# Kernel optimization log

Measured on AMD Instinct MI355X. Metric: run time of the kernel, lower is better.

The kernel has to match this reference:

```python
import jax, jax.numpy as jnp
import numpy as np
import math

B, H, L = 8, 256, 4096
C = 1            # channels
D_STATE = 64
DD = D_STATE // 2  # d = 32
DT_MIN, DT_MAX = 1e-3, 1e-1


def setup_inputs() -> dict:
    key = jax.random.key(0)
    ks = jax.random.split(key, 6)
    u = jax.random.normal(ks[0], (B, H, L), dtype=jnp.float32)
    # analytic init matching the torch module
    h_scale = jnp.exp(jnp.arange(H, dtype=jnp.float32) / H * math.log(DT_MAX / DT_MIN))  # (H,)
    angles = jnp.arange(DD, dtype=jnp.float32) * jnp.float32(np.pi)                      # (DD,)
    theta = jnp.einsum('c,h,d->chd', jnp.ones((C,), jnp.float32), h_scale, angles)       # (C,H,DD)
    a = -jnp.broadcast_to(h_scale[None, :, None], (C, H, DD)).astype(jnp.float32)        # (C,H,DD)
    D = jax.random.normal(ks[1], (C, H), dtype=jnp.float32)
    b_p = jax.random.normal(ks[2], (C, H, DD), dtype=jnp.float32)
    c_p = jax.random.normal(ks[3], (C, H, DD), dtype=jnp.float32)
    x0 = jax.random.normal(ks[4], (C, H, DD), dtype=jnp.float32)
    return {"u": u, "theta": theta, "a": a, "D": D, "b_p": b_p, "c_p": c_p, "x0": x0}


def fft_conv(u, f):
    # u: (B,H,L), f: (C,H,L) -> (B,C,H,L) causal conv via zero-padded FFT
    l = u.shape[-1]
    n = 2 * l
    u_f = jnp.fft.rfft(u, n=n)          # (B,H,n//2+1)
    f_f = jnp.fft.rfft(f, n=n)          # (C,H,n//2+1)
    y_f = jnp.einsum('bhl,chl->bchl', u_f, f_f)
    return jnp.fft.irfft(y_f, n=n)[..., :l]


def reference(u, theta, a, D, b_p, c_p, x0):
    l = u.shape[-1]
    T = 1.0 / (l - 1)
    zk = T * jnp.arange(l, dtype=jnp.float32)            # (L,)
    zk4 = zk[None, None, :, None]                         # (1,1,L,1)
    ls = -jnp.abs(a) + 1j * theta                         # (C,H,DD) complex
    term_0 = (jnp.exp(ls * T) - 1.0) / ls                 # (C,H,DD)
    # base_term: (C,H,L,DD)
    base_term = (2.0 * term_0[:, :, None, :] * jnp.exp(ls[:, :, None, :] * zk4)).real
    q = b_p * c_p                                         # (C,H,DD)
    f = jnp.einsum('chd,chld->chl', q, base_term)         # (C,H,L)
    y = fft_conv(u, f)                                    # (B,C,H,L)
    y = y + jnp.einsum('bhl,ch->bchl', u, D)
    # initial-condition term
    cos_term = 2.0 * T * jnp.exp(-jnp.abs(a)[:, :, None, :] * zk4) * jnp.cos(theta[:, :, None, :] * zk4)
    init = jnp.einsum('chd,chld->chl', 2.0 * (c_p * x0), cos_term)  # (C,H,L)
    y = y + init[None]                                    # broadcast over batch
    b = y.shape[0]
    return y.reshape(b, -1, l)                            # (B, C*H, L)
```

## Files before the change

kernel.cpp:

```cpp
#include <hip/hip_runtime.h>

#define BB 8
#define HH 256
#define LL 4096
#define STR 72

#define WS_H  0
#define WS_P  (2u*1024*1024)
#define WS_R  (4u*1024*1024)
#define WS_C1 (6u*1024*1024)
#define WS_C2 (6u*1024*1024 + 128u*1024)

typedef __attribute__((ext_vector_type(8))) short short8;
typedef __attribute__((ext_vector_type(4))) float f32x4;

static __device__ inline unsigned short f2bf(float x) {
    union { float f; unsigned u; } v; v.f = x;
    unsigned r = v.u + 0x7fffu + ((v.u >> 16) & 1u);
    return (unsigned short)(r >> 16);
}
static __device__ inline float bf2f(unsigned short us) {
    union { unsigned u; float f; } v; v.u = ((unsigned)us) << 16; return v.f;
}

#define CMUL(or_, oi_, ar_, ai_, br_, bi_) do { \
    float _tr = fmaf((ar_), (br_), -(ai_) * (bi_)); \
    float _ti = fmaf((ar_), (bi_), (ai_) * (br_)); \
    (or_) = _tr; (oi_) = _ti; } while (0)

__global__ __launch_bounds__(256) void s4_pre_kernel(
    const float* __restrict__ theta, const float* __restrict__ a,
    const float* __restrict__ b_p,   const float* __restrict__ c_p,
    const float* __restrict__ x0,
    unsigned short* __restrict__ Hm, unsigned short* __restrict__ Pm,
    unsigned short* __restrict__ Rm, float4* __restrict__ C1,
    float* __restrict__ C2)
{
    const int tid = threadIdx.x;
    const int h   = blockIdx.x;
    const int d   = tid & 31;
    const int kb  = tid >> 5;
    const float T = 1.0f / (LL - 1);
    __shared__ float h_s[64];

    const float lr = a[h * 32 + d];
    const float li = theta[h * 32 + d];
    float sn, cS;
    sincosf(li * T, &sn, &cS);
    const float er = expf(lr * T);
    const float Rr = er * cS, Ri = er * sn;
    const float den = lr * lr + li * li;
    const float t0r = ((Rr - 1.f) * lr + Ri * li) / den;
    const float t0i = (Ri * lr - (Rr - 1.f) * li) / den;
    const float qq  = b_p[h * 32 + d] * c_p[h * 32 + d];
    const float wre = 2.f * qq * t0r, wim = 2.f * qq * t0i;
    const float vv  = 4.f * T * c_p[h * 32 + d] * x0[h * 32 + d];

    float r2r, r2i, r4r, r4i, r8r, r8i, r16r, r16i, r32r, r32i;
    CMUL(r2r, r2i, Rr, Ri, Rr, Ri);
    CMUL(r4r, r4i, r2r, r2i, r2r, r2i);
    CMUL(r8r, r8i, r4r, r4i, r4r, r4i);
    CMUL(r16r, r16i, r8r, r8i, r8r, r8i);
    CMUL(r32r, r32i, r16r, r16i, r16r, r16i);

    unsigned short* HmB = Hm + h * 4096;
    unsigned short* PmB = Pm + h * 4096;
    unsigned short* RmB = Rm + h * 4096;

    {
        float pr = 1.f, pi = 0.f;
        if (kb & 1) CMUL(pr, pi, pr, pi, r8r, r8i);
        if (kb & 2) CMUL(pr, pi, pr, pi, r16r, r16i);
        if (kb & 4) CMUL(pr, pi, pr, pi, r32r, r32i);
        #pragma unroll
        for (int k8 = 0; k8 < 8; ++k8) {
            const int k = (kb << 3) + k8;
            RmB[k * 64 + d]           = f2bf(pr);
            RmB[k * 64 + 32 + d]      = f2bf(-pi);
            PmB[d * 64 + (63 - k)]        = f2bf(pr);
            PmB[(32 + d) * 64 + (63 - k)] = f2bf(pi);
            float hk = fmaf(wre, pr, -wim * pi);
            hk += __shfl_xor(hk, 1);
            hk += __shfl_xor(hk, 2);
            hk += __shfl_xor(hk, 4);
            hk += __shfl_xor(hk, 8);
            hk += __shfl_xor(hk, 16);
            if (d == 0) h_s[k] = hk;
            CMUL(pr, pi, pr, pi, Rr, Ri);
        }
    }
    if (tid < 32) {
        float Ar, Ai, wrr, wri;
        CMUL(Ar, Ai, r32r, r32i, r32r, r32i);
        CMUL(wrr, wri, wre, wim, Rr, Ri);
        C1[h * 32 + d] = make_float4(Ar, Ai, wrr, wri);
        C2[h * 32 + d] = vv;
    }
    __syncthreads();

    {
        const int t  = tid >> 2;
        const int tb = (tid & 3) << 4;
        #pragma unroll
        for (int g = 0; g < 4; ++g) {
            const int tau0 = tb + (g << 2);
            unsigned short e[4];
            #pragma unroll
            for (int i = 0; i < 4; ++i) {
                const int dt = t - (tau0 + i);
                e[i] = (dt >= 0) ? f2bf(h_s[dt]) : (unsigned short)0;
            }
            uint2 pk;
            pk.x = (unsigned)e[0] | ((unsigned)e[1] << 16);
            pk.y = (unsigned)e[2] | ((unsigned)e[3] << 16);
            *(uint2*)&HmB[t * 64 + tau0] = pk;
        }
    }
}

__global__ __launch_bounds__(256, 5) void s4_main_kernel(
    const float* __restrict__ u, const float* __restrict__ Dp,
    const unsigned short* __restrict__ Hm, const unsigned short* __restrict__ Pm,
    const unsigned short* __restrict__ Rm, const float4* __restrict__ C1,
    const float* __restrict__ C2, float* __restrict__ out)
{
    const int tid = threadIdx.x;
    const int bh  = blockIdx.x;
    const int hh  = bh & (HH - 1);

    __shared__ __align__(16) short Us[64 * STR];
    __shared__ __align__(16) short EQ[64 * STR];
    __shared__ __align__(16) float Seg[32 * 18];

    const float* up = u + ((size_t)bh << 12);
    #pragma unroll
    for (int jj = 0; jj < 4; ++jj) {
        const int v  = tid + (jj << 8);
        const float4 val = ((const float4*)up)[v];
        const int c  = v >> 4;
        const int t0 = (v & 15) << 2;
        uint2 pk;
        pk.x = (unsigned)f2bf(val.x) | ((unsigned)f2bf(val.y) << 16);
        pk.y = (unsigned)f2bf(val.z) | ((unsigned)f2bf(val.w) << 16);
        *(uint2*)&Us[c * STR + t0] = pk;
    }

    const int d = tid & 31;
    const int g = tid >> 5;
    const float4 c1 = C1[hh * 32 + d];
    const float vv  = C2[hh * 32 + d];
    const float Dh  = Dp[hh];
    __syncthreads();

    const int ln   = tid & 63;
    const int m0   = (tid >> 6) << 4;
    const int rowi = ln & 15;
    const int quad = ln >> 4;
    const unsigned short* HmB = Hm + hh * 4096;
    const unsigned short* PmB = Pm + hh * 4096;
    const unsigned short* RmB = Rm + hh * 4096;
    f32x4 accY[4], accE[4];
    #pragma unroll
    for (int nt = 0; nt < 4; ++nt) {
        accY[nt] = (f32x4){0.f, 0.f, 0.f, 0.f};
        accE[nt] = (f32x4){0.f, 0.f, 0.f, 0.f};
    }
    #pragma unroll
    for (int k0 = 0; k0 < 64; k0 += 32) {
        const short8 aH = *(const short8*)&HmB[(m0 + rowi) * 64 + k0 + (quad << 3)];
        const short8 aP = *(const short8*)&PmB[(m0 + rowi) * 64 + k0 + (quad << 3)];
        #pragma unroll
        for (int nt = 0; nt < 4; ++nt) {
            const short8 bU = *(const short8*)&Us[((nt << 4) + rowi) * STR + k0 + (quad << 3)];
            accY[nt] = __builtin_amdgcn_mfma_f32_16x16x32_bf16(aH, bU, accY[nt], 0, 0, 0);
            accE[nt] = __builtin_amdgcn_mfma_f32_16x16x32_bf16(aP, bU, accE[nt], 0, 0, 0);
        }
    }

    #pragma unroll
    for (int nt = 0; nt < 4; ++nt) {
        uint2 pk;
        pk.x = (unsigned)f2bf(accE[nt][0]) | ((unsigned)f2bf(accE[nt][1]) << 16);
        pk.y = (unsigned)f2bf(accE[nt][2]) | ((unsigned)f2bf(accE[nt][3]) << 16);
        *(uint2*)&EQ[((nt << 4) + rowi) * STR + m0 + (quad << 2)] = pk;
    }
    __syncthreads();

    const float Ar = c1.x, Ai = c1.y;
    float Er[8], Ei[8];
    {
        float Sr = 0.f, Si = 0.f;
        #pragma unroll
        for (int i = 0; i < 8; ++i) {
            const int c = (g << 3) + i;
            Er[i] = bf2f((unsigned short)EQ[c * STR + d]);
            Ei[i] = bf2f((unsigned short)EQ[c * STR + 32 + d]);
            const float nr = fmaf(Ar, Sr, fmaf(-Ai, Si, Er[i]));
            const float ni = fmaf(Ar, Si, fmaf(Ai, Sr, Ei[i]));
            Sr = nr; Si = ni;
        }
        Seg[d * 18 + (g << 1)]     = Sr;
        Seg[d * 18 + (g << 1) + 1] = Si;
    }
    __syncthreads();

    {
        float S8r, S8i, S16r, S16i, S32r, S32i;
        float b1r, b1i, b2r, b2i;
        CMUL(b1r, b1i, Ar, Ai, Ar, Ai);
        CMUL(b2r, b2i, b1r, b1i, b1r, b1i);
        CMUL(S8r, S8i, b2r, b2i, b2r, b2i);
        CMUL(S16r, S16i, S8r, S8i, S8r, S8i);
        CMUL(S32r, S32i, S16r, S16i, S16r, S16i);
        float offr = 0.f, offi = 0.f;
        #pragma unroll
        for (int gp = 0; gp < 7; ++gp) {
            const float2 sg = *(const float2*)&Seg[d * 18 + (gp << 1)];
            const float nr = fmaf(S8r, offr, fmaf(-S8i, offi, sg.x));
            const float ni = fmaf(S8r, offi, fmaf(S8i, offr, sg.y));
            const bool take = gp < g;
            offr = take ? nr : offr;
            offi = take ? ni : offi;
        }
        float Gr = vv, Gi = 0.f;
        if (g & 1) { float nr, ni; CMUL(nr, ni, Gr, Gi, S8r, S8i);   Gr = nr; Gi = ni; }
        if (g & 2) { float nr, ni; CMUL(nr, ni, Gr, Gi, S16r, S16i); Gr = nr; Gi = ni; }
        if (g & 4) { float nr, ni; CMUL(nr, ni, Gr, Gi, S32r, S32i); Gr = nr; Gi = ni; }
        const float wrr = c1.z, wri = c1.w;
        float Sr = offr, Si = offi;
        #pragma unroll
        for (int i = 0; i < 8; ++i) {
            const int c = (g << 3) + i;
            const float Qr = fmaf(wrr, Sr, fmaf(-wri, Si, Gr));
            const float Qi = fmaf(wrr, Si, fmaf(wri, Sr, Gi));
            EQ[c * STR + d]      = (short)f2bf(Qr);
            EQ[c * STR + 32 + d] = (short)f2bf(Qi);
            const float nr = fmaf(Ar, Sr, fmaf(-Ai, Si, Er[i]));
            const float ni = fmaf(Ar, Si, fmaf(Ai, Sr, Ei[i]));
            Sr = nr; Si = ni;
            float nGr, nGi;
            CMUL(nGr, nGi, Ar, Ai, Gr, Gi);
            Gr = nGr; Gi = nGi;
        }
    }
    __syncthreads();

    #pragma unroll
    for (int k0 = 0; k0 < 64; k0 += 32) {
        const short8 aR = *(const short8*)&RmB[(m0 + rowi) * 64 + k0 + (quad << 3)];
        #pragma unroll
        for (int nt = 0; nt < 4; ++nt) {
            const short8 bQ = *(const short8*)&EQ[((nt << 4) + rowi) * STR + k0 + (quad << 3)];
            accY[nt] = __builtin_amdgcn_mfma_f32_16x16x32_bf16(aR, bQ, accY[nt], 0, 0, 0);
        }
    }

    float* op = out + ((size_t)bh << 12);
    #pragma unroll
    for (int nt = 0; nt < 4; ++nt) {
        const int c    = (nt << 4) + rowi;
        const int toff = m0 + (quad << 2);
        const uint2 uu = *(const uint2*)&Us[c * STR + toff];
        float4 res;
        res.x = fmaf(Dh, bf2f((unsigned short)(uu.x & 0xffffu)), accY[nt][0]);
        res.y = fmaf(Dh, bf2f((unsigned short)(uu.x >> 16)),     accY[nt][1]);
        res.z = fmaf(Dh, bf2f((unsigned short)(uu.y & 0xffffu)), accY[nt][2]);
        res.w = fmaf(Dh, bf2f((unsigned short)(uu.y >> 16)),     accY[nt][3]);
        *(float4*)&op[c * 64 + toff] = res;
    }
}

extern "C" void kernel_launch(void* const* d_in, const int* in_sizes, int n_in,
                              void* d_out, int out_size, void* d_ws, size_t ws_size,
                              hipStream_t stream) {
    const float* u     = (const float*)d_in[0];
    const float* theta = (const float*)d_in[1];
    const float* a     = (const float*)d_in[2];
    const float* Dp    = (const float*)d_in[3];
    const float* b_p   = (const float*)d_in[4];
    const float* c_p   = (const float*)d_in[5];
    const float* x0    = (const float*)d_in[6];
    float* out = (float*)d_out;
    char* ws = (char*)d_ws;
    unsigned short* Hm = (unsigned short*)(ws + WS_H);
    unsigned short* Pm = (unsigned short*)(ws + WS_P);
    unsigned short* Rm = (unsigned short*)(ws + WS_R);
    float4*         C1 = (float4*)(ws + WS_C1);
    float*          C2 = (float*)(ws + WS_C2);

    hipLaunchKernelGGL(s4_pre_kernel, dim3(HH), dim3(256), 0, stream,
                       theta, a, b_p, c_p, x0, Hm, Pm, Rm, C1, C2);
    hipLaunchKernelGGL(s4_main_kernel, dim3(BB * HH), dim3(256), 0, stream,
                       u, Dp, Hm, Pm, Rm, C1, C2, out);
}
```

Before: 105.1 us.

## Process two batch rows per block, reuse H/P/R fragments and prefetch second input

```diff
diff --git a/kernel.cpp b/kernel.cpp
--- a/kernel.cpp
+++ b/kernel.cpp
@@ -118,155 +118,193 @@
     }
 }
 
-__global__ __launch_bounds__(256, 5) void s4_main_kernel(
+__global__ __launch_bounds__(256, 4) void s4_main_kernel(
     const float* __restrict__ u, const float* __restrict__ Dp,
     const unsigned short* __restrict__ Hm, const unsigned short* __restrict__ Pm,
     const unsigned short* __restrict__ Rm, const float4* __restrict__ C1,
     const float* __restrict__ C2, float* __restrict__ out)
 {
     const int tid = threadIdx.x;
-    const int bh  = blockIdx.x;
-    const int hh  = bh & (HH - 1);
-
-    __shared__ __align__(16) short Us[64 * STR];
+    const int blk = blockIdx.x;
+    const int hh  = blk >> 2;
+    const int bp  = blk & 3;
+
+    __shared__ __align__(16) short UsA[64 * STR];
+    __shared__ __align__(16) short UsB[64 * STR];
     __shared__ __align__(16) short EQ[64 * STR];
     __shared__ __align__(16) float Seg[32 * 18];
 
-    const float* up = u + ((size_t)bh << 12);
+    const int d    = tid & 31;
+    const int g    = tid >> 5;
+    const int ln   = tid & 63;
+    const int m0   = (tid >> 6) << 4;
+    const int rowi = ln & 15;
+    const int quad = ln >> 4;
+
+    const unsigned short* HmB = Hm + hh * 4096;
+    const unsigned short* PmB = Pm + hh * 4096;
+    const unsigned short* RmB = Rm + hh * 4096;
+    short8 aH[2], aP[2], aR[2];
+    #pragma unroll
+    for (int kh = 0; kh < 2; ++kh) {
+        const int off = (m0 + rowi) * 64 + (kh << 5) + (quad << 3);
+        aH[kh] = *(const short8*)&HmB[off];
+        aP[kh] = *(const short8*)&PmB[off];
+        aR[kh] = *(const short8*)&RmB[off];
+    }
+
+    const float* up0 = u + ((((size_t)(bp * 2) * HH) + hh) << 12);
+    const float* up1 = u + ((((size_t)(bp * 2 + 1) * HH) + hh) << 12);
     #pragma unroll
     for (int jj = 0; jj < 4; ++jj) {
         const int v  = tid + (jj << 8);
-        const float4 val = ((const float4*)up)[v];
+        const float4 val = ((const float4*)up0)[v];
         const int c  = v >> 4;
         const int t0 = (v & 15) << 2;
         uint2 pk;
         pk.x = (unsigned)f2bf(val.x) | ((unsigned)f2bf(val.y) << 16);
         pk.y = (unsigned)f2bf(val.z) | ((unsigned)f2bf(val.w) << 16);
-        *(uint2*)&Us[c * STR + t0] = pk;
-    }
-
-    const int d = tid & 31;
-    const int g = tid >> 5;
+        *(uint2*)&UsA[c * STR + t0] = pk;
+    }
+    float4 v1[4];
+    #pragma unroll
+    for (int jj = 0; jj < 4; ++jj)
+        v1[jj] = ((const float4*)up1)[tid + (jj << 8)];
+
     const float4 c1 = C1[hh * 32 + d];
     const float vv  = C2[hh * 32 + d];
     const float Dh  = Dp[hh];
-    __syncthreads();
-
-    const int ln   = tid & 63;
-    const int m0   = (tid >> 6) << 4;
-    const int rowi = ln & 15;
-    const int quad = ln >> 4;
-    const unsigned short* HmB = Hm + hh * 4096;
-    const unsigned short* PmB = Pm + hh * 4096;
-    const unsigned short* RmB = Rm + hh * 4096;
-    f32x4 accY[4], accE[4];
-    #pragma unroll
-    for (int nt = 0; nt < 4; ++nt) {
-        accY[nt] = (f32x4){0.f, 0.f, 0.f, 0.f};
-        accE[nt] = (f32x4){0.f, 0.f, 0.f, 0.f};
-    }
-    #pragma unroll
-    for (int k0 = 0; k0 < 64; k0 += 32) {
-        const short8 aH = *(const short8*)&HmB[(m0 + rowi) * 64 + k0 + (quad << 3)];
-        const short8 aP = *(const short8*)&PmB[(m0 + rowi) * 64 + k0 + (quad << 3)];
-        #pragma unroll
-        for (int nt = 0; nt < 4; ++nt) {
-            const short8 bU = *(const short8*)&Us[((nt << 4) + rowi) * STR + k0 + (quad << 3)];
-            accY[nt] = __builtin_amdgcn_mfma_f32_16x16x32_bf16(aH, bU, accY[nt], 0, 0, 0);
-            accE[nt] = __builtin_amdgcn_mfma_f32_16x16x32_bf16(aP, bU, accE[nt], 0, 0, 0);
-        }
-    }
-
-    #pragma unroll
-    for (int nt = 0; nt < 4; ++nt) {
-        uint2 pk;
-        pk.x = (unsigned)f2bf(accE[nt][0]) | ((unsigned)f2bf(accE[nt][1]) << 16);
-        pk.y = (unsigned)f2bf(accE[nt][2]) | ((unsigned)f2bf(accE[nt][3]) << 16);
-        *(uint2*)&EQ[((nt << 4) + rowi) * STR + m0 + (quad << 2)] = pk;
-    }
-    __syncthreads();
-
     const float Ar = c1.x, Ai = c1.y;
-    float Er[8], Ei[8];
+    float S8r, S8i, S16r, S16i, S32r, S32i;
     {
-        float Sr = 0.f, Si = 0.f;
-        #pragma unroll
-        for (int i = 0; i < 8; ++i) {
-            const int c = (g << 3) + i;
-            Er[i] = bf2f((unsigned short)EQ[c * STR + d]);
-            Ei[i] = bf2f((unsigned short)EQ[c * STR + 32 + d]);
-            const float nr = fmaf(Ar, Sr, fmaf(-Ai, Si, Er[i]));
-            const float ni = fmaf(Ar, Si, fmaf(Ai, Sr, Ei[i]));
-            Sr = nr; Si = ni;
-        }
-        Seg[d * 18 + (g << 1)]     = Sr;
-        Seg[d * 18 + (g << 1) + 1] = Si;
-    }
-    __syncthreads();
-
-    {
-        float S8r, S8i, S16r, S16i, S32r, S32i;
         float b1r, b1i, b2r, b2i;
         CMUL(b1r, b1i, Ar, Ai, Ar, Ai);
         CMUL(b2r, b2i, b1r, b1i, b1r, b1i);
         CMUL(S8r, S8i, b2r, b2i, b2r, b2i);
         CMUL(S16r, S16i, S8r, S8i, S8r, S8i);
         CMUL(S32r, S32i, S16r, S16i, S16r, S16i);
-        float offr = 0.f, offi = 0.f;
-        #pragma unroll
-        for (int gp = 0; gp < 7; ++gp) {
-            const float2 sg = *(const float2*)&Seg[d * 18 + (gp << 1)];
-            const float nr = fmaf(S8r, offr, fmaf(-S8i, offi, sg.x));
-            const float ni = fmaf(S8r, offi, fmaf(S8i, offr, sg.y));
-            const bool take = gp < g;
-            offr = take ? nr : offr;
-            offi = take ? ni : offi;
-        }
-        float Gr = vv, Gi = 0.f;
-        if (g & 1) { float nr, ni; CMUL(nr, ni, Gr, Gi, S8r, S8i);   Gr = nr; Gi = ni; }
-        if (g & 2) { float nr, ni; CMUL(nr, ni, Gr, Gi, S16r, S16i); Gr = nr; Gi = ni; }
-        if (g & 4) { float nr, ni; CMUL(nr, ni, Gr, Gi, S32r, S32i); Gr = nr; Gi = ni; }
-        const float wrr = c1.z, wri = c1.w;
-        float Sr = offr, Si = offi;
-        #pragma unroll
-        for (int i = 0; i < 8; ++i) {
-            const int c = (g << 3) + i;
-            const float Qr = fmaf(wrr, Sr, fmaf(-wri, Si, Gr));
-            const float Qi = fmaf(wrr, Si, fmaf(wri, Sr, Gi));
-            EQ[c * STR + d]      = (short)f2bf(Qr);
-            EQ[c * STR + 32 + d] = (short)f2bf(Qi);
-            const float nr = fmaf(Ar, Sr, fmaf(-Ai, Si, Er[i]));
-            const float ni = fmaf(Ar, Si, fmaf(Ai, Sr, Ei[i]));
-            Sr = nr; Si = ni;
-            float nGr, nGi;
-            CMUL(nGr, nGi, Ar, Ai, Gr, Gi);
-            Gr = nGr; Gi = nGi;
-        }
     }
     __syncthreads();
 
     #pragma unroll
-    for (int k0 = 0; k0 < 64; k0 += 32) {
-        const short8 aR = *(const short8*)&RmB[(m0 + rowi) * 64 + k0 + (quad << 3)];
+    for (int it = 0; it < 2; ++it) {
+        short* Us = it ? UsB : UsA;
+
+        f32x4 accY[4], accE[4];
         #pragma unroll
         for (int nt = 0; nt < 4; ++nt) {
-            const short8 bQ = *(const short8*)&EQ[((nt << 4) + rowi) * STR + k0 + (quad << 3)];
-            accY[nt] = __builtin_amdgcn_mfma_f32_16x16x32_bf16(aR, bQ, accY[nt], 0, 0, 0);
-        }
-    }
-
-    float* op = out + ((size_t)bh << 12);
-    #pragma unroll
-    for (int nt = 0; nt < 4; ++nt) {
-        const int c    = (nt << 4) + rowi;
-        const int toff = m0 + (quad << 2);
-        const uint2 uu = *(const uint2*)&Us[c * STR + toff];
-        float4 res;
-        res.x = fmaf(Dh, bf2f((unsigned short)(uu.x & 0xffffu)), accY[nt][0]);
-        res.y = fmaf(Dh, bf2f((unsigned short)(uu.x >> 16)),     accY[nt][1]);
-        res.z = fmaf(Dh, bf2f((unsigned short)(uu.y & 0xffffu)), accY[nt][2]);
-        res.w = fmaf(Dh, bf2f((unsigned short)(uu.y >> 16)),     accY[nt][3]);
-        *(float4*)&op[c * 64 + toff] = res;
+            accY[nt] = (f32x4){0.f, 0.f, 0.f, 0.f};
+            accE[nt] = (f32x4){0.f, 0.f, 0.f, 0.f};
+        }
+        #pragma unroll
+        for (int kh = 0; kh < 2; ++kh) {
+            const int k0 = kh << 5;
+            #pragma unroll
+            for (int nt = 0; nt < 4; ++nt) {
+                const short8 bU = *(const short8*)&Us[((nt << 4) + rowi) * STR + k0 + (quad << 3)];
+                accY[nt] = __builtin_amdgcn_mfma_f32_16x16x32_bf16(aH[kh], bU, accY[nt], 0, 0, 0);
+                accE[nt] = __builtin_amdgcn_mfma_f32_16x16x32_bf16(aP[kh], bU, accE[nt], 0, 0, 0);
+            }
+        }
+
+        #pragma unroll
+        for (int nt = 0; nt < 4; ++nt) {
+            uint2 pk;
+            pk.x = (unsigned)f2bf(accE[nt][0]) | ((unsigned)f2bf(accE[nt][1]) << 16);
+            pk.y = (unsigned)f2bf(accE[nt][2]) | ((unsigned)f2bf(accE[nt][3]) << 16);
+            *(uint2*)&EQ[((nt << 4) + rowi) * STR + m0 + (quad << 2)] = pk;
+        }
+
+        if (it == 0) {
+            #pragma unroll
+            for (int jj = 0; jj < 4; ++jj) {
+                const int v  = tid + (jj << 8);
+                const int c  = v >> 4;
+                const int t0 = (v & 15) << 2;
+                uint2 pk;
+                pk.x = (unsigned)f2bf(v1[jj].x) | ((unsigned)f2bf(v1[jj].y) << 16);
+                pk.y = (unsigned)f2bf(v1[jj].z) | ((unsigned)f2bf(v1[jj].w) << 16);
+                *(uint2*)&UsB[c * STR + t0] = pk;
+            }
+        }
+        __syncthreads();
+
+        const int cb = g << 3;
+        float Er[8], Ei[8];
+        {
+            float Sr = 0.f, Si = 0.f;
+            #pragma unroll
+            for (int i = 0; i < 8; ++i) {
+                const int c = cb + i;
+                Er[i] = bf2f((unsigned short)EQ[c * STR + d]);
+                Ei[i] = bf2f((unsigned short)EQ[c * STR + 32 + d]);
+                const float nr = fmaf(Ar, Sr, fmaf(-Ai, Si, Er[i]));
+                const float ni = fmaf(Ar, Si, fmaf(Ai, Sr, Ei[i]));
+                Sr = nr; Si = ni;
+            }
+            Seg[d * 18 + (g << 1)]     = Sr;
+            Seg[d * 18 + (g << 1) + 1] = Si;
+        }
+        __syncthreads();
+
+        {
+            float offr = 0.f, offi = 0.f;
+            #pragma unroll
+            for (int gp = 0; gp < 7; ++gp) {
+                const float2 sg = *(const float2*)&Seg[d * 18 + (gp << 1)];
+                const float nr = fmaf(S8r, offr, fmaf(-S8i, offi, sg.x));
+                const float ni = fmaf(S8r, offi, fmaf(S8i, offr, sg.y));
+                const bool take = gp < g;
+                offr = take ? nr : offr;
+                offi = take ? ni : offi;
+            }
+            float Gr = vv, Gi = 0.f;
+            if (g & 1) { float nr, ni; CMUL(nr, ni, Gr, Gi, S8r, S8i);   Gr = nr; Gi = ni; }
+            if (g & 2) { float nr, ni; CMUL(nr, ni, Gr, Gi, S16r, S16i); Gr = nr; Gi = ni; }
+            if (g & 4) { float nr, ni; CMUL(nr, ni, Gr, Gi, S32r, S32i); Gr = nr; Gi = ni; }
+            const float wrr = c1.z, wri = c1.w;
+            float Sr = offr, Si = offi;
+            #pragma unroll
+            for (int i = 0; i < 8; ++i) {
+                const int c = cb + i;
+                const float Qr = fmaf(wrr, Sr, fmaf(-wri, Si, Gr));
+                const float Qi = fmaf(wrr, Si, fmaf(wri, Sr, Gi));
+                EQ[c * STR + d]      = (short)f2bf(Qr);
+                EQ[c * STR + 32 + d] = (short)f2bf(Qi);
+                const float nr = fmaf(Ar, Sr, fmaf(-Ai, Si, Er[i]));
+                const float ni = fmaf(Ar, Si, fmaf(Ai, Sr, Ei[i]));
+                Sr = nr; Si = ni;
+                float nGr, nGi;
+                CMUL(nGr, nGi, Ar, Ai, Gr, Gi);
+                Gr = nGr; Gi = nGi;
+            }
+        }
+        __syncthreads();
+
+        #pragma unroll
+        for (int kh = 0; kh < 2; ++kh) {
+            const int k0 = kh << 5;
+            #pragma unroll
+            for (int nt = 0; nt < 4; ++nt) {
+                const short8 bQ = *(const short8*)&EQ[((nt << 4) + rowi) * STR + k0 + (quad << 3)];
+                accY[nt] = __builtin_amdgcn_mfma_f32_16x16x32_bf16(aR[kh], bQ, accY[nt], 0, 0, 0);
+            }
+        }
+
+        float* op = out + ((((size_t)(bp * 2 + it) * HH) + hh) << 12);
+        #pragma unroll
+        for (int nt = 0; nt < 4; ++nt) {
+            const int c    = (nt << 4) + rowi;
+            const int toff = m0 + (quad << 2);
+            const uint2 uu = *(const uint2*)&Us[c * STR + toff];
+            float4 res;
+            res.x = fmaf(Dh, bf2f((unsigned short)(uu.x & 0xffffu)), accY[nt][0]);
+            res.y = fmaf(Dh, bf2f((unsigned short)(uu.x >> 16)),     accY[nt][1]);
+            res.z = fmaf(Dh, bf2f((unsigned short)(uu.y & 0xffffu)), accY[nt][2]);
+            res.w = fmaf(Dh, bf2f((unsigned short)(uu.y >> 16)),     accY[nt][3]);
+            *(float4*)&op[c * 64 + toff] = res;
+        }
+        __syncthreads();
     }
 }
 
@@ -290,6 +328,6 @@
 
     hipLaunchKernelGGL(s4_pre_kernel, dim3(HH), dim3(256), 0, stream,
                        theta, a, b_p, c_p, x0, Hm, Pm, Rm, C1, C2);
-    hipLaunchKernelGGL(s4_main_kernel, dim3(BB * HH), dim3(256), 0, stream,
+    hipLaunchKernelGGL(s4_main_kernel, dim3(HH * 4), dim3(256), 0, stream,
                        u, Dp, Hm, Pm, Rm, C1, C2, out);
 }
```

After: 104.6 us. No clear change (-0.5%).

## Map one wavefront per (batch, head) sequence and fold D skip into Toeplitz diagonal

Applied to the files above, without the earlier changes.

```diff
diff --git a/kernel.cpp b/kernel.cpp
--- a/kernel.cpp
+++ b/kernel.cpp
@@ -1,6 +1,5 @@
 #include <hip/hip_runtime.h>
 
-#define BB 8
 #define HH 256
 #define LL 4096
 #define STR 72
@@ -31,7 +30,7 @@
 __global__ __launch_bounds__(256) void s4_pre_kernel(
     const float* __restrict__ theta, const float* __restrict__ a,
     const float* __restrict__ b_p,   const float* __restrict__ c_p,
-    const float* __restrict__ x0,
+    const float* __restrict__ x0,    const float* __restrict__ Dp,
     unsigned short* __restrict__ Hm, unsigned short* __restrict__ Pm,
     unsigned short* __restrict__ Rm, float4* __restrict__ C1,
     float* __restrict__ C2)
@@ -45,6 +44,7 @@
 
     const float lr = a[h * 32 + d];
     const float li = theta[h * 32 + d];
+    const float Dh = Dp[h];
     float sn, cS;
     sincosf(li * T, &sn, &cS);
     const float er = expf(lr * T);
@@ -75,8 +75,8 @@
         #pragma unroll
         for (int k8 = 0; k8 < 8; ++k8) {
             const int k = (kb << 3) + k8;
-            RmB[k * 64 + d]           = f2bf(pr);
-            RmB[k * 64 + 32 + d]      = f2bf(-pi);
+            RmB[k * 64 + (d << 1)]     = f2bf(pr);
+            RmB[k * 64 + (d << 1) + 1] = f2bf(-pi);
             PmB[d * 64 + (63 - k)]        = f2bf(pr);
             PmB[(32 + d) * 64 + (63 - k)] = f2bf(pi);
             float hk = fmaf(wre, pr, -wim * pi);
@@ -85,7 +85,7 @@
             hk += __shfl_xor(hk, 4);
             hk += __shfl_xor(hk, 8);
             hk += __shfl_xor(hk, 16);
-            if (d == 0) h_s[k] = hk;
+            if (d == 0) h_s[k] = hk + ((k == 0) ? Dh : 0.f);
             CMUL(pr, pi, pr, pi, Rr, Ri);
         }
     }
@@ -118,156 +118,161 @@
     }
 }
 
-__global__ __launch_bounds__(256, 5) void s4_main_kernel(
-    const float* __restrict__ u, const float* __restrict__ Dp,
+__global__ __launch_bounds__(256, 2) void s4_main_kernel(
+    const float* __restrict__ u,
     const unsigned short* __restrict__ Hm, const unsigned short* __restrict__ Pm,
     const unsigned short* __restrict__ Rm, const float4* __restrict__ C1,
     const float* __restrict__ C2, float* __restrict__ out)
 {
-    const int tid = threadIdx.x;
-    const int bh  = blockIdx.x;
-    const int hh  = bh & (HH - 1);
-
-    __shared__ __align__(16) short Us[64 * STR];
-    __shared__ __align__(16) short EQ[64 * STR];
-    __shared__ __align__(16) float Seg[32 * 18];
-
-    const float* up = u + ((size_t)bh << 12);
-    #pragma unroll
-    for (int jj = 0; jj < 4; ++jj) {
-        const int v  = tid + (jj << 8);
-        const float4 val = ((const float4*)up)[v];
-        const int c  = v >> 4;
-        const int t0 = (v & 15) << 2;
-        uint2 pk;
-        pk.x = (unsigned)f2bf(val.x) | ((unsigned)f2bf(val.y) << 16);
-        pk.y = (unsigned)f2bf(val.z) | ((unsigned)f2bf(val.w) << 16);
-        *(uint2*)&Us[c * STR + t0] = pk;
-    }
-
-    const int d = tid & 31;
-    const int g = tid >> 5;
+    const int tid   = threadIdx.x;
+    const int ln    = tid & 63;
+    const int wslot = tid >> 6;
+    const int wv    = (blockIdx.x << 2) + wslot;
+    const int hh    = wv >> 3;
+    const int b     = wv & 7;
+    const int rowi  = ln & 15;
+    const int quad  = ln >> 4;
+    const int d     = ln & 31;
+    const int half  = ln >> 5;
+
+    __shared__ __align__(16) short lds[4 * 64 * STR];
+    short* Tt = lds + wslot * (64 * STR);
+
     const float4 c1 = C1[hh * 32 + d];
     const float vv  = C2[hh * 32 + d];
-    const float Dh  = Dp[hh];
-    __syncthreads();
-
-    const int ln   = tid & 63;
-    const int m0   = (tid >> 6) << 4;
-    const int rowi = ln & 15;
-    const int quad = ln >> 4;
+
+    const float* up = u + (((size_t)(b * HH + hh)) << 12);
+    #pragma unroll
+    for (int j0 = 0; j0 < 16; j0 += 4) {
+        float4 vl[4];
+        #pragma unroll
+        for (int jj = 0; jj < 4; ++jj)
+            vl[jj] = ((const float4*)up)[ln + ((j0 + jj) << 6)];
+        #pragma unroll
+        for (int jj = 0; jj < 4; ++jj) {
+            const int v  = ln + ((j0 + jj) << 6);
+            const int c  = v >> 4;
+            const int t0 = (v & 15) << 2;
+            uint2 pk;
+            pk.x = (unsigned)f2bf(vl[jj].x) | ((unsigned)f2bf(vl[jj].y) << 16);
+            pk.y = (unsigned)f2bf(vl[jj].z) | ((unsigned)f2bf(vl[jj].w) << 16);
+            *(uint2*)&Tt[c * STR + t0] = pk;
+        }
+    }
+
     const unsigned short* HmB = Hm + hh * 4096;
     const unsigned short* PmB = Pm + hh * 4096;
     const unsigned short* RmB = Rm + hh * 4096;
-    f32x4 accY[4], accE[4];
-    #pragma unroll
-    for (int nt = 0; nt < 4; ++nt) {
-        accY[nt] = (f32x4){0.f, 0.f, 0.f, 0.f};
-        accE[nt] = (f32x4){0.f, 0.f, 0.f, 0.f};
-    }
-    #pragma unroll
-    for (int k0 = 0; k0 < 64; k0 += 32) {
-        const short8 aH = *(const short8*)&HmB[(m0 + rowi) * 64 + k0 + (quad << 3)];
-        const short8 aP = *(const short8*)&PmB[(m0 + rowi) * 64 + k0 + (quad << 3)];
+    f32x4 accY[4][4], accE[4][4];
+    #pragma unroll
+    for (int mt = 0; mt < 4; ++mt)
         #pragma unroll
         for (int nt = 0; nt < 4; ++nt) {
-            const short8 bU = *(const short8*)&Us[((nt << 4) + rowi) * STR + k0 + (quad << 3)];
-            accY[nt] = __builtin_amdgcn_mfma_f32_16x16x32_bf16(aH, bU, accY[nt], 0, 0, 0);
-            accE[nt] = __builtin_amdgcn_mfma_f32_16x16x32_bf16(aP, bU, accE[nt], 0, 0, 0);
-        }
-    }
-
-    #pragma unroll
-    for (int nt = 0; nt < 4; ++nt) {
-        uint2 pk;
-        pk.x = (unsigned)f2bf(accE[nt][0]) | ((unsigned)f2bf(accE[nt][1]) << 16);
-        pk.y = (unsigned)f2bf(accE[nt][2]) | ((unsigned)f2bf(accE[nt][3]) << 16);
-        *(uint2*)&EQ[((nt << 4) + rowi) * STR + m0 + (quad << 2)] = pk;
-    }
-    __syncthreads();
-
-    const float Ar = c1.x, Ai = c1.y;
-    float Er[8], Ei[8];
-    {
-        float Sr = 0.f, Si = 0.f;
-        #pragma unroll
-        for (int i = 0; i < 8; ++i) {
-            const int c = (g << 3) + i;
-            Er[i] = bf2f((unsigned short)EQ[c * STR + d]);
-            Ei[i] = bf2f((unsigned short)EQ[c * STR + 32 + d]);
-            const float nr = fmaf(Ar, Sr, fmaf(-Ai, Si, Er[i]));
-            const float ni = fmaf(Ar, Si, fmaf(Ai, Sr, Ei[i]));
-            Sr = nr; Si = ni;
-        }
-        Seg[d * 18 + (g << 1)]     = Sr;
-        Seg[d * 18 + (g << 1) + 1] = Si;
-    }
-    __syncthreads();
-
-    {
-        float S8r, S8i, S16r, S16i, S32r, S32i;
-        float b1r, b1i, b2r, b2i;
-        CMUL(b1r, b1i, Ar, Ai, Ar, Ai);
-        CMUL(b2r, b2i, b1r, b1i, b1r, b1i);
-        CMUL(S8r, S8i, b2r, b2i, b2r, b2i);
-        CMUL(S16r, S16i, S8r, S8i, S8r, S8i);
-        CMUL(S32r, S32i, S16r, S16i, S16r, S16i);
-        float offr = 0.f, offi = 0.f;
-        #pragma unroll
-        for (int gp = 0; gp < 7; ++gp) {
-            const float2 sg = *(const float2*)&Seg[d * 18 + (gp << 1)];
-            const float nr = fmaf(S8r, offr, fmaf(-S8i, offi, sg.x));
-            const float ni = fmaf(S8r, offi, fmaf(S8i, offr, sg.y));
-            const bool take = gp < g;
-            offr = take ? nr : offr;
-            offi = take ? ni : offi;
-        }
-        float Gr = vv, Gi = 0.f;
-        if (g & 1) { float nr, ni; CMUL(nr, ni, Gr, Gi, S8r, S8i);   Gr = nr; Gi = ni; }
-        if (g & 2) { float nr, ni; CMUL(nr, ni, Gr, Gi, S16r, S16i); Gr = nr; Gi = ni; }
-        if (g & 4) { float nr, ni; CMUL(nr, ni, Gr, Gi, S32r, S32i); Gr = nr; Gi = ni; }
-        const float wrr = c1.z, wri = c1.w;
-        float Sr = offr, Si = offi;
-        #pragma unroll
-        for (int i = 0; i < 8; ++i) {
-            const int c = (g << 3) + i;
-            const float Qr = fmaf(wrr, Sr, fmaf(-wri, Si, Gr));
-            const float Qi = fmaf(wrr, Si, fmaf(wri, Sr, Gi));
-            EQ[c * STR + d]      = (short)f2bf(Qr);
-            EQ[c * STR + 32 + d] = (short)f2bf(Qi);
-            const float nr = fmaf(Ar, Sr, fmaf(-Ai, Si, Er[i]));
-            const float ni = fmaf(Ar, Si, fmaf(Ai, Sr, Ei[i]));
-            Sr = nr; Si = ni;
-            float nGr, nGi;
-            CMUL(nGr, nGi, Ar, Ai, Gr, Gi);
-            Gr = nGr; Gi = nGi;
-        }
-    }
-    __syncthreads();
-
-    #pragma unroll
-    for (int k0 = 0; k0 < 64; k0 += 32) {
-        const short8 aR = *(const short8*)&RmB[(m0 + rowi) * 64 + k0 + (quad << 3)];
+            accY[mt][nt] = (f32x4){0.f, 0.f, 0.f, 0.f};
+            accE[mt][nt] = (f32x4){0.f, 0.f, 0.f, 0.f};
+        }
+    #pragma unroll
+    for (int kh = 0; kh < 2; ++kh) {
+        short8 bU[4];
+        #pragma unroll
+        for (int nt = 0; nt < 4; ++nt)
+            bU[nt] = *(const short8*)&Tt[((nt << 4) + rowi) * STR + (kh << 5) + (quad << 3)];
+        #pragma unroll
+        for (int mt = 0; mt < 4; ++mt) {
+            const int aoff = ((mt << 4) + rowi) * 64 + (kh << 5) + (quad << 3);
+            const short8 aH = *(const short8*)&HmB[aoff];
+            const short8 aP = *(const short8*)&PmB[aoff];
+            #pragma unroll
+            for (int nt = 0; nt < 4; ++nt) {
+                accY[mt][nt] = __builtin_amdgcn_mfma_f32_16x16x32_bf16(aH, bU[nt], accY[mt][nt], 0, 0, 0);
+                accE[mt][nt] = __builtin_amdgcn_mfma_f32_16x16x32_bf16(aP, bU[nt], accE[mt][nt], 0, 0, 0);
+            }
+        }
+    }
+    __builtin_amdgcn_wave_barrier();
+
+    #pragma unroll
+    for (int mt = 0; mt < 2; ++mt)
+        #pragma unroll
+        for (int nt = 0; nt < 4; ++nt)
+            #pragma unroll
+            for (int i = 0; i < 4; ++i) {
+                const int dd = (mt << 4) + (quad << 2) + i;
+                const int c  = (nt << 4) + rowi;
+                const unsigned pk = (unsigned)f2bf(accE[mt][nt][i])
+                                  | ((unsigned)f2bf(accE[mt + 2][nt][i]) << 16);
+                *(unsigned*)&Tt[c * STR + (dd << 1)] = pk;
+            }
+    __builtin_amdgcn_wave_barrier();
+
+    const float Ar = c1.x, Ai = c1.y, wrr = c1.z, wri = c1.w;
+    float Sr = 0.f, Si = 0.f;
+    #pragma unroll
+    for (int i = 0; i < 32; ++i) {
+        const unsigned ee = *(const unsigned*)&Tt[((half << 5) + i) * STR + (d << 1)];
+        const float er_ = bf2f((unsigned short)(ee & 0xffffu));
+        const float ei_ = bf2f((unsigned short)(ee >> 16));
+        const float nr = fmaf(Ar, Sr, fmaf(-Ai, Si, er_));
+        const float ni = fmaf(Ar, Si, fmaf(Ai, Sr, ei_));
+        Sr = nr; Si = ni;
+    }
+    const float s0r = __shfl(Sr, d);
+    const float s0i = __shfl(Si, d);
+    float A5r = Ar, A5i = Ai;
+    #pragma unroll
+    for (int s = 0; s < 5; ++s) {
+        const float nr = A5r * A5r - A5i * A5i;
+        const float ni = 2.f * A5r * A5i;
+        A5r = nr; A5i = ni;
+    }
+    float Gr = half ? vv * A5r : vv;
+    float Gi = half ? vv * A5i : 0.f;
+    float Zr = half ? s0r : 0.f;
+    float Zi = half ? s0i : 0.f;
+    #pragma unroll
+    for (int i = 0; i < 32; ++i) {
+        const int crow = ((half << 5) + i) * STR + (d << 1);
+        const unsigned ee = *(const unsigned*)&Tt[crow];
+        const float er_ = bf2f((unsigned short)(ee & 0xffffu));
+        const float ei_ = bf2f((unsigned short)(ee >> 16));
+        const float Qr = fmaf(wrr, Zr, fmaf(-wri, Zi, Gr));
+        const float Qi = fmaf(wrr, Zi, fmaf(wri, Zr, Gi));
+        const unsigned pk = (unsigned)f2bf(Qr) | ((unsigned)f2bf(Qi) << 16);
+        *(unsigned*)&Tt[crow] = pk;
+        const float nr = fmaf(Ar, Zr, fmaf(-Ai, Zi, er_));
+        const float ni = fmaf(Ar, Zi, fmaf(Ai, Zr, ei_));
+        Zr = nr; Zi = ni;
+        float nGr, nGi;
+        CMUL(nGr, nGi, Ar, Ai, Gr, Gi);
+        Gr = nGr; Gi = nGi;
+    }
+    __builtin_amdgcn_wave_barrier();
+
+    #pragma unroll
+    for (int kh = 0; kh < 2; ++kh) {
+        short8 bQ[4];
+        #pragma unroll
+        for (int nt = 0; nt < 4; ++nt)
+            bQ[nt] = *(const short8*)&Tt[((nt << 4) + rowi) * STR + (kh << 5) + (quad << 3)];
+        #pragma unroll
+        for (int mt = 0; mt < 4; ++mt) {
+            const short8 aR = *(const short8*)&RmB[((mt << 4) + rowi) * 64 + (kh << 5) + (quad << 3)];
+            #pragma unroll
+            for (int nt = 0; nt < 4; ++nt)
+                accY[mt][nt] = __builtin_amdgcn_mfma_f32_16x16x32_bf16(aR, bQ[nt], accY[mt][nt], 0, 0, 0);
+        }
+    }
+
+    float* op = out + (((size_t)(b * HH + hh)) << 12);
+    #pragma unroll
+    for (int mt = 0; mt < 4; ++mt)
         #pragma unroll
         for (int nt = 0; nt < 4; ++nt) {
-            const short8 bQ = *(const short8*)&EQ[((nt << 4) + rowi) * STR + k0 + (quad << 3)];
-            accY[nt] = __builtin_amdgcn_mfma_f32_16x16x32_bf16(aR, bQ, accY[nt], 0, 0, 0);
-        }
-    }
-
-    float* op = out + ((size_t)bh << 12);
-    #pragma unroll
-    for (int nt = 0; nt < 4; ++nt) {
-        const int c    = (nt << 4) + rowi;
-        const int toff = m0 + (quad << 2);
-        const uint2 uu = *(const uint2*)&Us[c * STR + toff];
-        float4 res;
-        res.x = fmaf(Dh, bf2f((unsigned short)(uu.x & 0xffffu)), accY[nt][0]);
-        res.y = fmaf(Dh, bf2f((unsigned short)(uu.x >> 16)),     accY[nt][1]);
-        res.z = fmaf(Dh, bf2f((unsigned short)(uu.y & 0xffffu)), accY[nt][2]);
-        res.w = fmaf(Dh, bf2f((unsigned short)(uu.y >> 16)),     accY[nt][3]);
-        *(float4*)&op[c * 64 + toff] = res;
-    }
+            const int c = (nt << 4) + rowi;
+            const int k = (mt << 4) + (quad << 2);
+            *(float4*)&op[c * 64 + k] = make_float4(accY[mt][nt][0], accY[mt][nt][1],
+                                                    accY[mt][nt][2], accY[mt][nt][3]);
+        }
 }
 
 extern "C" void kernel_launch(void* const* d_in, const int* in_sizes, int n_in,
@@ -289,7 +294,7 @@
     float*          C2 = (float*)(ws + WS_C2);
 
     hipLaunchKernelGGL(s4_pre_kernel, dim3(HH), dim3(256), 0, stream,
-                       theta, a, b_p, c_p, x0, Hm, Pm, Rm, C1, C2);
-    hipLaunchKernelGGL(s4_main_kernel, dim3(BB * HH), dim3(256), 0, stream,
-                       u, Dp, Hm, Pm, Rm, C1, C2, out);
-}
+                       theta, a, b_p, c_p, x0, Dp, Hm, Pm, Rm, C1, C2);
+    hipLaunchKernelGGL(s4_main_kernel, dim3(512), dim3(256), 0, stream,
+                       u, Hm, Pm, Rm, C1, C2, out);
+}
```

Measured after the change: 108.2 us. 1.03x slower.
